# Kernel tuning notes

Hardware: AMD Instinct MI355X
Metric: run time of the kernel (lower is better)

## Reference

```python
import jax, jax.numpy as jnp
import numpy as np

PI = float(np.pi)

def setup_inputs() -> dict:
    key = jax.random.key(0)
    k1, k2 = jax.random.split(key)
    B, S, NUM_CHARS, P = 8, 8192, 95, 8
    char_idx = jax.random.randint(k1, (B, S), 0, NUM_CHARS, dtype=jnp.int32)
    positions = jnp.arange(S, dtype=jnp.int32)
    W = jax.random.normal(k2, (NUM_CHARS, P), dtype=jnp.float32)
    return {"char_idx": char_idx, "positions": positions, "W": W}

def reference(char_idx, positions, W):
    """Vectorized PhysicalTokenizer.encode (learnable Phase 2, eval mode).
    char_idx: [B,S] int, already offset by ascii_start; W: [num_chars,8].
    Returns quaternion tensor [B, S, embed_dim, 4].
    """
    embed_dim = 128
    params = W[char_idx]                                  # [B,S,8] gather
    omega = params[..., 0:1] * 2.0                        # [B,S,1]
    A1, A2, A3 = params[..., 1:2], params[..., 2:3], params[..., 3:4]
    beta = params[..., 4:5]
    gamma = jax.nn.sigmoid(params[..., 5:6])
    phi = params[..., 6:7] * PI
    j = jnp.arange(embed_dim, dtype=jnp.float32)          # [D]
    # spectral wave synthesis, fused elementwise over [B,S,D]
    wave = (A1 * jnp.sin(omega * j + phi)
            + A2 * jnp.sin(2.0 * omega * j + 2.0 * phi)
            + A3 * jnp.sin(3.0 * omega * j + 3.0 * phi)) * jnp.exp(-gamma * j)
    pos_phase = jnp.sin(positions.astype(jnp.float32) * (0.1 * PI))  # [S]
    wave = wave + beta * j * pos_phase[None, :, None]     # [B,S,D]
    psi0 = wave
    psi1 = jnp.roll(wave, shift=1, axis=-1)
    psi2 = jnp.sin(wave)
    psi3 = jnp.cos(wave)
    return jnp.stack([psi0, psi1, psi2, psi3], axis=-1)   # [B,S,D,4]
```

## Files before the change

### kernel.cpp

```cpp
#include <hip/hip_runtime.h>

#define PI_F 3.14159265358979323846f

constexpr int ED = 128;
constexpr int ROWS_PER_BLOCK = 4;

__global__ __launch_bounds__(256) void ptok_kernel(
    const int* __restrict__ char_idx,
    const int* __restrict__ positions,
    const float* __restrict__ W,
    float* __restrict__ out,
    int S)
{
    const int lane = threadIdx.x & 63;
    const int wv = threadIdx.x >> 6;
    const int row = blockIdx.x * ROWS_PER_BLOCK + wv;
    const int s = row & (S - 1);

    const int c = char_idx[row];
    const float4 p0 = reinterpret_cast<const float4*>(W + c * 8)[0];
    const float4 p1 = reinterpret_cast<const float4*>(W + c * 8)[1];
    const float omega = p0.x * 2.0f;
    const float A1 = p0.y, A2 = p0.z, A3 = p0.w;
    const float beta = p1.x;
    const float gamma = 1.0f / (1.0f + __expf(-p1.y));
    const float phi = p1.z * PI_F;

    const float pos_phase = __sinf((float)positions[s] * (0.1f * PI_F));

    float w01[2];
    #pragma unroll
    for (int k = 0; k < 2; ++k) {
        const float fj = (float)(lane + 64 * k);
        const float a = omega * fj + phi;
        const float sa = __sinf(a);
        const float ca = __cosf(a);
        const float wave = (A1 * sa + A2 * (2.0f * sa * ca)
                            + A3 * sa * (3.0f - 4.0f * sa * sa))
                           * __expf(-gamma * fj);
        w01[k] = wave + beta * fj * pos_phase;
    }

    const int lm1 = (lane + 63) & 63;
    const float u0 = __shfl(w01[0], lm1, 64);
    const float u1 = __shfl(w01[1], lm1, 64);
    const float prev0 = (lane == 0) ? u1 : u0;
    const float prev1 = (lane == 0) ? u0 : u1;

    float4* orow = reinterpret_cast<float4*>(out) + (size_t)row * ED;
    float4 o0, o1;
    o0.x = w01[0]; o0.y = prev0; o0.z = __sinf(w01[0]); o0.w = __cosf(w01[0]);
    o1.x = w01[1]; o1.y = prev1; o1.z = __sinf(w01[1]); o1.w = __cosf(w01[1]);
    orow[lane] = o0;
    orow[64 + lane] = o1;
}

extern "C" void kernel_launch(void* const* d_in, const int* in_sizes, int n_in,
                              void* d_out, int out_size, void* d_ws, size_t ws_size,
                              hipStream_t stream) {
    const int* char_idx  = (const int*)d_in[0];
    const int* positions = (const int*)d_in[1];
    const float* W       = (const float*)d_in[2];
    float* out = (float*)d_out;

    const int nrows = in_sizes[0];
    const int S = in_sizes[1];

    const int grid = nrows / ROWS_PER_BLOCK;
    ptok_kernel<<<grid, 256, 0, stream>>>(char_idx, positions, W, out, S);
}
```

Measured before the change: 26.40 us.

## Use persistent grid-stride waves with scalarized row index and FMA-folded wave math

Replaces the one-row-per-wave grid with a fixed grid of 2048 blocks whose waves loop over rows in grid-stride order. The row index goes through readfirstlane so per-row parameter loads can be scalar, and the wave arithmetic is rewritten with explicit fmaf and prefolded constants. The position is reduced modulo 20 before the sine, which uses the period of sin(0.1*pi*p) to keep the argument small for the fast sine. The aim is to cut block launch overhead and per-row vector work on a kernel limited by writing its output. The cost is less latency hiding per wave.

```diff
diff --git a/kernel.cpp b/kernel.cpp
--- a/kernel.cpp
+++ b/kernel.cpp
@@ -2,57 +2,64 @@
 
 #define PI_F 3.14159265358979323846f
 
-constexpr int ED = 128;
-constexpr int ROWS_PER_BLOCK = 4;
+constexpr int WPB = 4;
 
-__global__ __launch_bounds__(256) void ptok_kernel(
+typedef float f4 __attribute__((ext_vector_type(4)));
+
+__global__ __launch_bounds__(256) void ptok_persist(
     const int* __restrict__ char_idx,
     const int* __restrict__ positions,
     const float* __restrict__ W,
-    float* __restrict__ out,
-    int S)
+    f4* __restrict__ out,
+    int S, int nrows, int nwaves)
 {
     const int lane = threadIdx.x & 63;
-    const int wv = threadIdx.x >> 6;
-    const int row = blockIdx.x * ROWS_PER_BLOCK + wv;
-    const int s = row & (S - 1);
+    const int wid0 = __builtin_amdgcn_readfirstlane(
+        blockIdx.x * WPB + (threadIdx.x >> 6));
+    const float fj = (float)lane;
+    const int lm1 = (lane + 63) & 63;
 
-    const int c = char_idx[row];
-    const float4 p0 = reinterpret_cast<const float4*>(W + c * 8)[0];
-    const float4 p1 = reinterpret_cast<const float4*>(W + c * 8)[1];
-    const float omega = p0.x * 2.0f;
-    const float A1 = p0.y, A2 = p0.z, A3 = p0.w;
-    const float beta = p1.x;
-    const float gamma = 1.0f / (1.0f + __expf(-p1.y));
-    const float phi = p1.z * PI_F;
+    for (int row = wid0; row < nrows; row += nwaves) {
+        const int s = row & (S - 1);
+        const int c = char_idx[row];
+        const unsigned pv = (unsigned)positions[s];
+        const float pp = __sinf((float)(pv % 20u) * (0.1f * PI_F));
 
-    const float pos_phase = __sinf((float)positions[s] * (0.1f * PI_F));
+        const float* p = W + c * 8;
+        const float omega = p[0] * 2.0f;
+        const float A1 = p[1];
+        const float A2p = 2.0f * p[2];
+        const float A3 = p[3];
+        const float bp = p[4] * pp;
+        const float g = 1.0f / (1.0f + __expf(-p[5]));
+        const float phi = p[6] * PI_F;
 
-    float w01[2];
-    #pragma unroll
-    for (int k = 0; k < 2; ++k) {
-        const float fj = (float)(lane + 64 * k);
-        const float a = omega * fj + phi;
-        const float sa = __sinf(a);
-        const float ca = __cosf(a);
-        const float wave = (A1 * sa + A2 * (2.0f * sa * ca)
-                            + A3 * sa * (3.0f - 4.0f * sa * sa))
-                           * __expf(-gamma * fj);
-        w01[k] = wave + beta * fj * pos_phase;
+        float w[2];
+        #pragma unroll
+        for (int k = 0; k < 2; ++k) {
+            const float j = fj + 64.0f * k;
+            const float a = fmaf(omega, j, phi);
+            const float sa = __sinf(a);
+            const float ca = __cosf(a);
+            const float env = __expf(-g * j);
+            float acc = A1 * sa;
+            acc = fmaf(A2p, sa * ca, acc);
+            acc = fmaf(A3, sa * fmaf(-4.0f, sa * sa, 3.0f), acc);
+            w[k] = fmaf(bp, j, acc * env);
+        }
+
+        const float u0 = __shfl(w[0], lm1, 64);
+        const float u1 = __shfl(w[1], lm1, 64);
+        const float prev0 = (lane == 0) ? u1 : u0;
+        const float prev1 = (lane == 0) ? u0 : u1;
+
+        f4* orow = out + ((size_t)row << 7);
+        f4 o0, o1;
+        o0.x = w[0]; o0.y = prev0; o0.z = __sinf(w[0]); o0.w = __cosf(w[0]);
+        o1.x = w[1]; o1.y = prev1; o1.z = __sinf(w[1]); o1.w = __cosf(w[1]);
+        orow[lane] = o0;
+        orow[64 + lane] = o1;
     }
-
-    const int lm1 = (lane + 63) & 63;
-    const float u0 = __shfl(w01[0], lm1, 64);
-    const float u1 = __shfl(w01[1], lm1, 64);
-    const float prev0 = (lane == 0) ? u1 : u0;
-    const float prev1 = (lane == 0) ? u0 : u1;
-
-    float4* orow = reinterpret_cast<float4*>(out) + (size_t)row * ED;
-    float4 o0, o1;
-    o0.x = w01[0]; o0.y = prev0; o0.z = __sinf(w01[0]); o0.w = __cosf(w01[0]);
-    o1.x = w01[1]; o1.y = prev1; o1.z = __sinf(w01[1]); o1.w = __cosf(w01[1]);
-    orow[lane] = o0;
-    orow[64 + lane] = o1;
 }
 
 extern "C" void kernel_launch(void* const* d_in, const int* in_sizes, int n_in,
@@ -61,11 +68,12 @@
     const int* char_idx  = (const int*)d_in[0];
     const int* positions = (const int*)d_in[1];
     const float* W       = (const float*)d_in[2];
-    float* out = (float*)d_out;
 
     const int nrows = in_sizes[0];
     const int S = in_sizes[1];
 
-    const int grid = nrows / ROWS_PER_BLOCK;
-    ptok_kernel<<<grid, 256, 0, stream>>>(char_idx, positions, W, out, S);
+    const int nblocks = 2048;
+    const int nwaves = nblocks * WPB;
+    ptok_persist<<<nblocks, 256, 0, stream>>>(
+        char_idx, positions, W, (f4*)d_out, S, nrows, nwaves);
 }
```

Result: no change. 26.64 us (+0.9%).
